# Kernel optimization log

Measured on AMD Instinct MI355X. Metric: run time of the kernel, lower is better.

## Reference

```python
import jax, jax.numpy as jnp
import numpy as np

DT_MIN, DT_MAX = 1e-3, 0.1
DT_RANK, D_STATE = 64, 16


def setup_inputs() -> dict:
    key = jax.random.key(0)
    ks = jax.random.split(key, 8)
    B, L, D_MODEL, D_INNER = 2, 4096, 1024, 2048
    s = 0.02
    return {
        "x": jax.random.normal(ks[0], (B, L, D_MODEL), jnp.float32),
        "W_in": jax.random.normal(ks[1], (D_MODEL, 2 * D_INNER), jnp.float32) * s,
        "W_xproj": jax.random.normal(ks[2], (D_INNER, DT_RANK + 2 * D_STATE), jnp.float32) * s,
        "W_dt": jax.random.normal(ks[3], (DT_RANK, D_INNER), jnp.float32) * s,
        "b_dt": jax.random.normal(ks[4], (D_INNER,), jnp.float32) * s,
        "A_log": jnp.log(jax.random.uniform(ks[5], (D_INNER, D_STATE), jnp.float32) + 0.5),
        "D": jnp.ones((D_INNER,), jnp.float32),
        "W_out": jax.random.normal(ks[6], (D_INNER, D_MODEL), jnp.float32) * s,
    }


def _selective_scan(xp, delta, A, Bm, Cm):
    # xp, delta: [B, L, d_inner]; Bm, Cm: [B, L, d_state]; A: [d_inner, d_state]
    batch, L, d_inner = xp.shape
    d_state = A.shape[1]

    def step(h, inp):
        x_t, dt_t, B_t, C_t = inp  # [B,di], [B,di], [B,ds], [B,ds]
        A_bar = 1.0 + A[None] * dt_t[..., None]            # [B, di, ds]
        B_bar = B_t[:, None, :] * dt_t[..., None]          # [B, di, ds]
        h = A_bar * h + B_bar * x_t[..., None]             # [B, di, ds]
        y_t = jnp.sum(C_t[:, None, :] * h, axis=-1)        # [B, di]
        return h, y_t

    h0 = jnp.zeros((batch, d_inner, d_state), xp.dtype)
    xs = (
        jnp.swapaxes(xp, 0, 1),
        jnp.swapaxes(delta, 0, 1),
        jnp.swapaxes(Bm, 0, 1),
        jnp.swapaxes(Cm, 0, 1),
    )
    _, ys = jax.lax.scan(step, h0, xs)  # ys: [L, B, d_inner]
    return jnp.swapaxes(ys, 0, 1)


def reference(x, W_in, W_xproj, W_dt, b_dt, A_log, D, W_out):
    xz = x @ W_in
    xp, z = jnp.split(xz, 2, axis=-1)                      # [B,L,d_inner] each
    x_dbl = xp @ W_xproj
    dlt, Bm, Cm = jnp.split(x_dbl, [DT_RANK, DT_RANK + D_STATE], axis=-1)
    delta = jnp.clip(jax.nn.softplus(dlt @ W_dt + b_dt), DT_MIN, DT_MAX)
    A = -jnp.exp(A_log)
    y = _selective_scan(xp, delta, A, Bm, Cm)
    y = y + D[None, None, :] * xp
    y = y * jax.nn.silu(z)
    return y @ W_out
```

## Files before the change

### kernel.cpp

```cpp
#include <hip/hip_runtime.h>
#include <cstdint>
#include <cstddef>

typedef unsigned short u16;
typedef __attribute__((ext_vector_type(8))) short bf16x8;
typedef __attribute__((ext_vector_type(4))) float f32x4;

__device__ __forceinline__ float bf2f(u16 u) {
  unsigned v = ((unsigned)u) << 16;
  return __builtin_bit_cast(float, v);
}
__device__ __forceinline__ u16 f2bf(float f) {
  unsigned u = __builtin_bit_cast(unsigned, f);
  u = (u + 0x7FFFu + ((u >> 16) & 1u)) >> 16;
  return (u16)u;
}

__device__ __forceinline__ void gload16(const void* g, void* l) {
  __builtin_amdgcn_global_load_lds(
      (const __attribute__((address_space(1))) void*)g,
      (__attribute__((address_space(3))) void*)l,
      16, 0, 0);
}

__global__ __launch_bounds__(256) void f32_to_bf16_kernel(
    const float* __restrict__ in, u16* __restrict__ out, int n) {
  int i = (blockIdx.x * 256 + threadIdx.x) * 4;
  if (i < n) {
    float4 v = *(const float4*)(in + i);
    ushort4 o;
    o.x = f2bf(v.x); o.y = f2bf(v.y); o.z = f2bf(v.z); o.w = f2bf(v.w);
    *(ushort4*)(out + i) = o;
  }
}

__global__ void transpose_f32_bf16T_kernel(
    const float* __restrict__ in, u16* __restrict__ out, int R, int C) {
  __shared__ float tile[32][33];
  const int bx = blockIdx.x * 32;
  const int by = blockIdx.y * 32;
  const int tx = threadIdx.x, ty = threadIdx.y;
#pragma unroll
  for (int i = 0; i < 32; i += 8)
    tile[ty + i][tx] = in[(size_t)(by + ty + i) * C + bx + tx];
  __syncthreads();
#pragma unroll
  for (int i = 0; i < 32; i += 8)
    out[(size_t)(bx + ty + i) * R + by + tx] = f2bf(tile[tx][ty + i]);
}

template <int BN, int NR, int EPI>
__global__ __launch_bounds__(256) void gemm_bt(
    const u16* __restrict__ A, const u16* __restrict__ Bt,
    int M, int N, int K,
    void* __restrict__ o0, void* __restrict__ o1, void* __restrict__ o2,
    const float* __restrict__ bias) {
  constexpr int BM = 128, BK = 32, MR = 4;
  __shared__ __align__(16) u16 As[BM * BK];
  __shared__ __align__(16) u16 Bs[BN * BK];
  const int tid = threadIdx.x;
  const int wid = tid >> 6, lane = tid & 63;
  const int wr = wid >> 1, wc = wid & 1;
  const int m0 = blockIdx.y * BM, n0 = blockIdx.x * BN;
  const int l16 = lane & 15, lk = lane >> 4;

  f32x4 acc[MR][NR];
#pragma unroll
  for (int m = 0; m < MR; ++m)
#pragma unroll
    for (int n = 0; n < NR; ++n) {
      f32x4 z = {0.f, 0.f, 0.f, 0.f};
      acc[m][n] = z;
    }

  constexpr int CH_A = (BM * BK * 2) / 1024;
  constexpr int CH_B = (BN * BK * 2) / 1024;

  for (int k0 = 0; k0 < K; k0 += BK) {
    for (int c = wid; c < CH_A; c += 4) {
      int off = c * 1024 + lane * 16;
      int e = off >> 1;
      int m = e >> 5, kk = e & 31;
      gload16(A + (size_t)(m0 + m) * K + (k0 + kk), (char*)As + off);
    }
    for (int c = wid; c < CH_B; c += 4) {
      int off = c * 1024 + lane * 16;
      int e = off >> 1;
      int n = e >> 5, kk = e & 31;
      gload16(Bt + (size_t)(n0 + n) * K + (k0 + kk), (char*)Bs + off);
    }
    __syncthreads();
    bf16x8 af[MR], bfr[NR];
#pragma unroll
    for (int m = 0; m < MR; ++m)
      af[m] = *(const bf16x8*)(As + (wr * 64 + m * 16 + l16) * BK + lk * 8);
#pragma unroll
    for (int n = 0; n < NR; ++n)
      bfr[n] = *(const bf16x8*)(Bs + (wc * (NR * 16) + n * 16 + l16) * BK + lk * 8);
#pragma unroll
    for (int m = 0; m < MR; ++m)
#pragma unroll
      for (int n = 0; n < NR; ++n)
        acc[m][n] = __builtin_amdgcn_mfma_f32_16x16x32_bf16(af[m], bfr[n], acc[m][n], 0, 0, 0);
    __syncthreads();
  }

#pragma unroll
  for (int m = 0; m < MR; ++m) {
#pragma unroll
    for (int n = 0; n < NR; ++n) {
#pragma unroll
      for (int r = 0; r < 4; ++r) {
        const int row = m0 + wr * 64 + m * 16 + (lane >> 4) * 4 + r;
        const int col = n0 + wc * (NR * 16) + n * 16 + (lane & 15);
        float v = acc[m][n][r];
        if constexpr (EPI == 0) {
          if (col < 2048) {
            ((u16*)o0)[(size_t)row * 2048 + col] = f2bf(v);
          } else {
            float sv = v / (1.f + __expf(-v));
            ((u16*)o1)[(size_t)row * 2048 + (col - 2048)] = f2bf(sv);
          }
        } else if constexpr (EPI == 1) {
          if (col < 64) {
            ((u16*)o0)[(size_t)row * 64 + col] = f2bf(v);
          } else if (col < 80) {
            ((float*)o1)[(size_t)row * 16 + (col - 64)] = v;
          } else {
            ((float*)o2)[(size_t)row * 16 + (col - 80)] = v;
          }
        } else if constexpr (EPI == 2) {
          v += bias[col];
          float sp = (v > 20.f) ? v : log1pf(__expf(v));
          sp = fminf(fmaxf(sp, 1e-3f), 0.1f);
          ((u16*)o0)[(size_t)row * 2048 + col] = f2bf(sp);
        } else {
          ((float*)o0)[(size_t)row * (size_t)N + col] = v;
        }
      }
    }
  }
}


template <int TC>
__global__ __launch_bounds__(256) void scan_pass1(
    const u16* __restrict__ xp, const u16* __restrict__ dt,
    const float* __restrict__ Bc, const float* __restrict__ A_log,
    float* __restrict__ P, float* __restrict__ Q, int NC) {
  const int di = blockIdx.x * 256 + threadIdx.x;
  const int c = blockIdx.y, b = blockIdx.z;
  __shared__ __align__(16) float Bs[TC * 16];
  {
    const float* src = Bc + (size_t)(b * 4096 + c * TC) * 16;
    for (int i = threadIdx.x; i < TC * 4; i += 256)
      *(float4*)(Bs + i * 4) = *(const float4*)(src + i * 4);
  }
  float A[16], h[16], Pp[16];
#pragma unroll
  for (int s = 0; s < 16; ++s) {
    A[s] = -__expf(A_log[di * 16 + s]);
    h[s] = 0.f;
    Pp[s] = 1.f;
  }
  __syncthreads();
  size_t gidx = (size_t)(b * 4096 + c * TC) * 2048 + di;
  for (int t = 0; t < TC; ++t, gidx += 2048) {
    float xv = bf2f(xp[gidx]), dv = bf2f(dt[gidx]);
    float dvx = dv * xv;
#pragma unroll
    for (int q = 0; q < 4; ++q) {
      f32x4 bv = ((const f32x4*)(Bs + t * 16))[q];
#pragma unroll
      for (int j = 0; j < 4; ++j) {
        int s = q * 4 + j;
        float abar = fmaf(A[s], dv, 1.f);
        h[s] = fmaf(abar, h[s], bv[j] * dvx);
        Pp[s] *= abar;
      }
    }
  }
  const size_t obase = ((size_t)(b * NC + c) * 16) * 2048 + di;
#pragma unroll
  for (int s = 0; s < 16; ++s) {
    P[obase + (size_t)s * 2048] = Pp[s];
    Q[obase + (size_t)s * 2048] = h[s];
  }
}

__global__ __launch_bounds__(256) void scan_pass2(
    const float* __restrict__ P, const float* __restrict__ Q,
    float* __restrict__ Hin, int NC) {
  const int di = blockIdx.x * 256 + threadIdx.x;
  const int s = blockIdx.y, b = blockIdx.z;
  float hin = 0.f;
  const size_t idx0 = ((size_t)(b * NC) * 16 + s) * 2048 + di;
#pragma unroll 8
  for (int c = 0; c < NC; ++c) {
    size_t idx = idx0 + (size_t)c * (16 * 2048);
    Hin[idx] = hin;
    hin = fmaf(P[idx], hin, Q[idx]);
  }
}

template <int TC>
__global__ __launch_bounds__(256) void scan_pass3(
    const u16* __restrict__ xp, const u16* __restrict__ dt,
    const u16* __restrict__ zs, const float* __restrict__ Bc,
    const float* __restrict__ Cc, const float* __restrict__ A_log,
    const float* __restrict__ Dv, const float* __restrict__ Hin,
    u16* __restrict__ Y, int NC) {
  const int di = blockIdx.x * 256 + threadIdx.x;
  const int c = blockIdx.y, b = blockIdx.z;
  __shared__ __align__(16) float Bs[TC * 16], Cs[TC * 16];
  {
    const float* srcB = Bc + (size_t)(b * 4096 + c * TC) * 16;
    const float* srcC = Cc + (size_t)(b * 4096 + c * TC) * 16;
    for (int i = threadIdx.x; i < TC * 4; i += 256) {
      *(float4*)(Bs + i * 4) = *(const float4*)(srcB + i * 4);
      *(float4*)(Cs + i * 4) = *(const float4*)(srcC + i * 4);
    }
  }
  float A[16], h[16];
  const size_t hbase = ((size_t)(b * NC + c) * 16) * 2048 + di;
#pragma unroll
  for (int s = 0; s < 16; ++s) {
    A[s] = -__expf(A_log[di * 16 + s]);
    h[s] = Hin[hbase + (size_t)s * 2048];
  }
  const float Dg = Dv[di];
  __syncthreads();
  size_t gidx = (size_t)(b * 4096 + c * TC) * 2048 + di;
  for (int t = 0; t < TC; ++t, gidx += 2048) {
    float xv = bf2f(xp[gidx]), dv = bf2f(dt[gidx]), zv = bf2f(zs[gidx]);
    float dvx = dv * xv;
    float y = 0.f;
#pragma unroll
    for (int q = 0; q < 4; ++q) {
      f32x4 bv = ((const f32x4*)(Bs + t * 16))[q];
      f32x4 cv = ((const f32x4*)(Cs + t * 16))[q];
#pragma unroll
      for (int j = 0; j < 4; ++j) {
        int s = q * 4 + j;
        float abar = fmaf(A[s], dv, 1.f);
        h[s] = fmaf(abar, h[s], bv[j] * dvx);
        y = fmaf(cv[j], h[s], y);
      }
    }
    float yo = fmaf(Dg, xv, y) * zv;
    Y[gidx] = f2bf(yo);
  }
}

extern "C" void kernel_launch(void* const* d_in, const int* in_sizes, int n_in,
                              void* d_out, int out_size, void* d_ws, size_t ws_size,
                              hipStream_t stream) {
  (void)in_sizes; (void)n_in; (void)out_size; (void)ws_size;
  const float* x       = (const float*)d_in[0];
  const float* W_in    = (const float*)d_in[1];
  const float* W_xproj = (const float*)d_in[2];
  const float* W_dt    = (const float*)d_in[3];
  const float* b_dt    = (const float*)d_in[4];
  const float* A_log   = (const float*)d_in[5];
  const float* Dv      = (const float*)d_in[6];
  const float* W_out   = (const float*)d_in[7];
  float* out = (float*)d_out;

  constexpr size_t MB = 1ull << 20;
  char* ws = (char*)d_ws;
  constexpr size_t O_XP    = 0;
  constexpr size_t O_ZS    = 32 * MB;
  constexpr size_t O_DELTA = 64 * MB;
  constexpr size_t O_BC    = 96 * MB;
  constexpr size_t O_CC    = O_BC + 512 * 1024;
  constexpr size_t O_WOUTT = 97 * MB;
  constexpr size_t O_Y     = 101 * MB;
  constexpr size_t O_XB    = 133 * MB;
  constexpr size_t O_WINT  = 149 * MB;
  constexpr size_t O_WXT   = 157 * MB;
  constexpr size_t O_WDTT  = O_WXT + 393216;
  constexpr size_t O_DLT   = O_WDTT + 262144;
  constexpr size_t O_P     = 133 * MB;
  constexpr size_t O_Q     = 149 * MB;
  constexpr size_t O_HIN   = 165 * MB;

  u16* xb    = (u16*)(ws + O_XB);
  u16* WinT  = (u16*)(ws + O_WINT);
  u16* WxT   = (u16*)(ws + O_WXT);
  u16* WdtT  = (u16*)(ws + O_WDTT);
  u16* WoutT = (u16*)(ws + O_WOUTT);
  u16* xpb   = (u16*)(ws + O_XP);
  u16* zsb   = (u16*)(ws + O_ZS);
  u16* dltb  = (u16*)(ws + O_DLT);
  float* Bcf = (float*)(ws + O_BC);
  float* Ccf = (float*)(ws + O_CC);
  u16* delb  = (u16*)(ws + O_DELTA);
  u16* Yb    = (u16*)(ws + O_Y);
  float* Pf  = (float*)(ws + O_P);
  float* Qf  = (float*)(ws + O_Q);
  float* Hin = (float*)(ws + O_HIN);

  dim3 tb(32, 8);
  f32_to_bf16_kernel<<<8192 * 1024 / 1024, 256, 0, stream>>>(x, xb, 8192 * 1024);
  transpose_f32_bf16T_kernel<<<dim3(4096 / 32, 1024 / 32), tb, 0, stream>>>(W_in, WinT, 1024, 4096);
  transpose_f32_bf16T_kernel<<<dim3(96 / 32, 2048 / 32), tb, 0, stream>>>(W_xproj, WxT, 2048, 96);
  transpose_f32_bf16T_kernel<<<dim3(2048 / 32, 64 / 32), tb, 0, stream>>>(W_dt, WdtT, 64, 2048);
  transpose_f32_bf16T_kernel<<<dim3(1024 / 32, 2048 / 32), tb, 0, stream>>>(W_out, WoutT, 2048, 1024);

  gemm_bt<128, 4, 0><<<dim3(4096 / 128, 8192 / 128), 256, 0, stream>>>(
      xb, WinT, 8192, 4096, 1024, xpb, zsb, nullptr, nullptr);
  gemm_bt<96, 3, 1><<<dim3(1, 8192 / 128), 256, 0, stream>>>(
      xpb, WxT, 8192, 96, 2048, dltb, Bcf, Ccf, nullptr);
  gemm_bt<128, 4, 2><<<dim3(2048 / 128, 8192 / 128), 256, 0, stream>>>(
      dltb, WdtT, 8192, 2048, 64, delb, nullptr, nullptr, b_dt);

  constexpr int NC = 64, TC = 64;
  scan_pass1<TC><<<dim3(8, NC, 2), 256, 0, stream>>>(
      xpb, delb, Bcf, A_log, Pf, Qf, NC);
  scan_pass2<<<dim3(8, 16, 2), 256, 0, stream>>>(Pf, Qf, Hin, NC);
  scan_pass3<TC><<<dim3(8, NC, 2), 256, 0, stream>>>(
      xpb, delb, zsb, Bcf, Ccf, A_log, Dv, Hin, Yb, NC);

  gemm_bt<128, 4, 3><<<dim3(1024 / 128, 8192 / 128), 256, 0, stream>>>(
      Yb, WoutT, 8192, 1024, 2048, out, nullptr, nullptr, nullptr);
}
```

Before: 392.0 us.

## Add 256-row double-buffered GEMM kernel for input and output projections

Introduces a new 512-thread GEMM with 256xBN tiles, BK=64, double-buffered LDS filled by direct global-to-LDS loads with an XOR swizzle, explicit vmcnt waits, and s_setprio around MFMA bursts. The block index is remapped across groups of 8 for better L2 locality. It replaces the generic 128-tile GEMM for the in-projection and out-projection, which are the largest matmuls. The aim is more reuse per tile and overlap of loads with compute. The cost is higher register and LDS pressure, and the output GEMM gets only 256 blocks, which may underfill the GPU.

```diff
diff --git a/kernel.cpp b/kernel.cpp
--- a/kernel.cpp
+++ b/kernel.cpp
@@ -22,6 +22,8 @@
       (__attribute__((address_space(3))) void*)l,
       16, 0, 0);
 }
+
+__device__ __forceinline__ int swz(int lb) { return lb ^ (((lb >> 9) & 1) << 5); }
 
 __global__ __launch_bounds__(256) void f32_to_bf16_kernel(
     const float* __restrict__ in, u16* __restrict__ out, int n) {
@@ -47,6 +49,178 @@
 #pragma unroll
   for (int i = 0; i < 32; i += 8)
     out[(size_t)(bx + ty + i) * R + by + tx] = f2bf(tile[tx][ty + i]);
+}
+
+template <int BN, int EPI>
+__global__ __launch_bounds__(512, 2) void gemm256(
+    const u16* __restrict__ Ap, const u16* __restrict__ Btp,
+    int M, int N, int K, int gx,
+    void* __restrict__ o0, void* __restrict__ o1) {
+  constexpr int NFR = BN / 64;
+  constexpr int NFH = NFR / 2;
+  constexpr int A_ISS = 4;
+  constexpr int B_ISS = BN / 64;
+  constexpr int WN = BN / 4;
+  constexpr int BUFSZ = 32768 + BN * 128;
+  __shared__ __align__(1024) char smem[2 * BUFSZ];
+
+  const int tid = threadIdx.x;
+  const int wid = tid >> 6, lane = tid & 63;
+  const int wr = wid >> 2, wc = wid & 3;
+  const int l16 = lane & 15, lk = lane >> 4;
+
+  const int nwg = gridDim.x, bid = blockIdx.x;
+  const int rb = (bid & 7) * (nwg >> 3) + (bid >> 3);
+  const int bx = rb % gx, by = rb / gx;
+  const int m0 = by * 256, n0 = bx * BN;
+
+  const u16* gA[A_ISS];
+  const u16* gB[B_ISS];
+#pragma unroll
+  for (int i = 0; i < A_ISS; ++i) {
+    int pb = i * 8192 + tid * 16;
+    int lb = swz(pb);
+    gA[i] = Ap + (size_t)(m0 + (lb >> 7)) * K + ((lb & 127) >> 1);
+  }
+#pragma unroll
+  for (int i = 0; i < B_ISS; ++i) {
+    int pb = i * 8192 + tid * 16;
+    int lb = swz(pb);
+    gB[i] = Btp + (size_t)(n0 + (lb >> 7)) * K + ((lb & 127) >> 1);
+  }
+
+  auto stage = [&](int kt, int bb) {
+    char* dst = smem + bb * BUFSZ + (wid << 10);
+#pragma unroll
+    for (int i = 0; i < A_ISS; ++i)
+      gload16(gA[i] + kt * 64, dst + i * 8192);
+#pragma unroll
+    for (int i = 0; i < B_ISS; ++i)
+      gload16(gB[i] + kt * 64, dst + 32768 + i * 8192);
+  };
+
+  auto offA = [&](int f, int kk) {
+    int lb = (wr * 128 + f * 16 + l16) * 128 + kk * 64 + lk * 16;
+    return swz(lb);
+  };
+  auto offB = [&](int n, int kk) {
+    int lb = (wc * WN + n * 16 + l16) * 128 + kk * 64 + lk * 16;
+    return swz(lb);
+  };
+
+  f32x4 acc[8][NFR];
+#pragma unroll
+  for (int f = 0; f < 8; ++f)
+#pragma unroll
+    for (int n = 0; n < NFR; ++n) {
+      f32x4 z = {0.f, 0.f, 0.f, 0.f};
+      acc[f][n] = z;
+    }
+
+  const int NT = K >> 6;
+  stage(0, 0);
+  stage(1, 1);
+
+  for (int kt = 0; kt < NT; ++kt) {
+    const char* bufA = smem + (kt & 1) * BUFSZ;
+    const char* bufB = bufA + 32768;
+    if (kt < NT - 1) {
+      if constexpr (B_ISS == 4) asm volatile("s_waitcnt vmcnt(8)" ::: "memory");
+      else                      asm volatile("s_waitcnt vmcnt(6)" ::: "memory");
+    } else {
+      asm volatile("s_waitcnt vmcnt(0)" ::: "memory");
+    }
+    __builtin_amdgcn_s_barrier();
+
+    bf16x8 af[4][2], bh[2][NFH][2];
+#pragma unroll
+    for (int j = 0; j < 4; ++j)
+#pragma unroll
+      for (int kk = 0; kk < 2; ++kk)
+        af[j][kk] = *(const bf16x8*)(bufA + offA(j, kk));
+#pragma unroll
+    for (int j = 0; j < NFH; ++j)
+#pragma unroll
+      for (int kk = 0; kk < 2; ++kk)
+        bh[0][j][kk] = *(const bf16x8*)(bufB + offB(j, kk));
+    __builtin_amdgcn_s_setprio(1);
+#pragma unroll
+    for (int j = 0; j < 4; ++j)
+#pragma unroll
+      for (int n2 = 0; n2 < NFH; ++n2)
+#pragma unroll
+        for (int kk = 0; kk < 2; ++kk)
+          acc[j][n2] = __builtin_amdgcn_mfma_f32_16x16x32_bf16(
+              af[j][kk], bh[0][n2][kk], acc[j][n2], 0, 0, 0);
+    __builtin_amdgcn_s_setprio(0);
+#pragma unroll
+    for (int j = 0; j < NFH; ++j)
+#pragma unroll
+      for (int kk = 0; kk < 2; ++kk)
+        bh[1][j][kk] = *(const bf16x8*)(bufB + offB(NFH + j, kk));
+    __builtin_amdgcn_s_setprio(1);
+#pragma unroll
+    for (int j = 0; j < 4; ++j)
+#pragma unroll
+      for (int n2 = 0; n2 < NFH; ++n2)
+#pragma unroll
+        for (int kk = 0; kk < 2; ++kk)
+          acc[j][NFH + n2] = __builtin_amdgcn_mfma_f32_16x16x32_bf16(
+              af[j][kk], bh[1][n2][kk], acc[j][NFH + n2], 0, 0, 0);
+    __builtin_amdgcn_s_setprio(0);
+#pragma unroll
+    for (int j = 0; j < 4; ++j)
+#pragma unroll
+      for (int kk = 0; kk < 2; ++kk)
+        af[j][kk] = *(const bf16x8*)(bufA + offA(4 + j, kk));
+    __builtin_amdgcn_s_setprio(1);
+#pragma unroll
+    for (int j = 0; j < 4; ++j)
+#pragma unroll
+      for (int n2 = 0; n2 < NFH; ++n2)
+#pragma unroll
+        for (int kk = 0; kk < 2; ++kk)
+          acc[4 + j][NFH + n2] = __builtin_amdgcn_mfma_f32_16x16x32_bf16(
+              af[j][kk], bh[1][n2][kk], acc[4 + j][NFH + n2], 0, 0, 0);
+    __builtin_amdgcn_s_setprio(0);
+    __builtin_amdgcn_s_setprio(1);
+#pragma unroll
+    for (int j = 0; j < 4; ++j)
+#pragma unroll
+      for (int n2 = 0; n2 < NFH; ++n2)
+#pragma unroll
+        for (int kk = 0; kk < 2; ++kk)
+          acc[4 + j][n2] = __builtin_amdgcn_mfma_f32_16x16x32_bf16(
+              af[j][kk], bh[0][n2][kk], acc[4 + j][n2], 0, 0, 0);
+    __builtin_amdgcn_s_setprio(0);
+
+    asm volatile("s_waitcnt lgkmcnt(0)" ::: "memory");
+    __builtin_amdgcn_s_barrier();
+    if (kt + 2 < NT) stage(kt + 2, kt & 1);
+  }
+
+#pragma unroll
+  for (int f = 0; f < 8; ++f) {
+#pragma unroll
+    for (int n = 0; n < NFR; ++n) {
+#pragma unroll
+      for (int rr = 0; rr < 4; ++rr) {
+        const int row = m0 + wr * 128 + f * 16 + lk * 4 + rr;
+        const int col = n0 + wc * WN + n * 16 + l16;
+        float v = acc[f][n][rr];
+        if constexpr (EPI == 0) {
+          if (col < 2048) {
+            ((u16*)o0)[(size_t)row * 2048 + col] = f2bf(v);
+          } else {
+            float sv = v / (1.f + __expf(-v));
+            ((u16*)o1)[(size_t)row * 2048 + (col - 2048)] = f2bf(sv);
+          }
+        } else {
+          ((float*)o0)[(size_t)row * (size_t)N + col] = v;
+        }
+      }
+    }
+  }
 }
 
 template <int BN, int NR, int EPI>
@@ -114,14 +288,7 @@
         const int row = m0 + wr * 64 + m * 16 + (lane >> 4) * 4 + r;
         const int col = n0 + wc * (NR * 16) + n * 16 + (lane & 15);
         float v = acc[m][n][r];
-        if constexpr (EPI == 0) {
-          if (col < 2048) {
-            ((u16*)o0)[(size_t)row * 2048 + col] = f2bf(v);
-          } else {
-            float sv = v / (1.f + __expf(-v));
-            ((u16*)o1)[(size_t)row * 2048 + (col - 2048)] = f2bf(sv);
-          }
-        } else if constexpr (EPI == 1) {
+        if constexpr (EPI == 1) {
           if (col < 64) {
             ((u16*)o0)[(size_t)row * 64 + col] = f2bf(v);
           } else if (col < 80) {
@@ -134,14 +301,11 @@
           float sp = (v > 20.f) ? v : log1pf(__expf(v));
           sp = fminf(fmaxf(sp, 1e-3f), 0.1f);
           ((u16*)o0)[(size_t)row * 2048 + col] = f2bf(sp);
-        } else {
-          ((float*)o0)[(size_t)row * (size_t)N + col] = v;
         }
       }
     }
   }
 }
-
 
 template <int TC>
 __global__ __launch_bounds__(256) void scan_pass1(
@@ -307,8 +471,8 @@
   transpose_f32_bf16T_kernel<<<dim3(2048 / 32, 64 / 32), tb, 0, stream>>>(W_dt, WdtT, 64, 2048);
   transpose_f32_bf16T_kernel<<<dim3(1024 / 32, 2048 / 32), tb, 0, stream>>>(W_out, WoutT, 2048, 1024);
 
-  gemm_bt<128, 4, 0><<<dim3(4096 / 128, 8192 / 128), 256, 0, stream>>>(
-      xb, WinT, 8192, 4096, 1024, xpb, zsb, nullptr, nullptr);
+  gemm256<256, 0><<<512, 512, 0, stream>>>(
+      xb, WinT, 8192, 4096, 1024, 16, xpb, zsb);
   gemm_bt<96, 3, 1><<<dim3(1, 8192 / 128), 256, 0, stream>>>(
       xpb, WxT, 8192, 96, 2048, dltb, Bcf, Ccf, nullptr);
   gemm_bt<128, 4, 2><<<dim3(2048 / 128, 8192 / 128), 256, 0, stream>>>(
@@ -321,6 +485,6 @@
   scan_pass3<TC><<<dim3(8, NC, 2), 256, 0, stream>>>(
       xpb, delb, zsb, Bcf, Ccf, A_log, Dv, Hin, Yb, NC);
 
-  gemm_bt<128, 4, 3><<<dim3(1024 / 128, 8192 / 128), 256, 0, stream>>>(
-      Yb, WoutT, 8192, 1024, 2048, out, nullptr, nullptr, nullptr);
-}
+  gemm256<128, 3><<<256, 512, 0, stream>>>(
+      Yb, WoutT, 8192, 1024, 2048, 8, out, nullptr);
+}
```

Result: faster. 361.1 us (-7.9%).
